# Optimization experiments

Measured on AMD Instinct MI355X. Metric: run time of the kernel, lower is better.

Reference implementation:

```python
import math
import jax, jax.numpy as jnp
import numpy as np

B, T, D = 512, 512, 256
ALPHA = 0.5
BETA = 0.9


def setup_inputs() -> dict:
    key = jax.random.key(0)
    ks = jax.random.split(key, 9)
    s = 1.0 / math.sqrt(D)
    return {
        "window_features": jax.random.normal(ks[0], (B, T, D), jnp.float32),
        "timestamps": jax.random.uniform(ks[1], (B, T), jnp.float32) * 86400.0 * 7,
        "prev_L": jax.random.normal(ks[2], (B, D), jnp.float32),
        "prev_M": jax.random.uniform(ks[3], (B, 1), jnp.float32),
        "pad_mask": jnp.zeros((B, T), jnp.bool_),
        "W_Q": jax.random.normal(ks[4], (D, D), jnp.float32) * s,
        "W_K": jax.random.normal(ks[5], (D, D), jnp.float32) * s,
        "W_V": jax.random.normal(ks[6], (D, D), jnp.float32) * s,
        "cls_w": jax.random.normal(ks[7], (1, 2 * D + 1), jnp.float32) * s,
        "cls_b": jnp.zeros((1,), jnp.float32),
    }


def reference(window_features, timestamps, prev_L, prev_M, pad_mask,
              W_Q, W_K, W_V, cls_w, cls_b):
    Bv, Tv, d = window_features.shape
    valid = ~pad_mask
    valid_f = valid.astype(window_features.dtype)              # [B,T]
    valid_count = jnp.clip(valid_f.sum(1, keepdims=True), 1.0)  # [B,1]

    # decay weights from recency (days)
    t_masked = jnp.where(pad_mask, -1e18, timestamps)
    t_max = t_masked.max(1, keepdims=True)                      # [B,1]
    dt = jnp.clip(t_max - timestamps, 0.0) / 86400.0
    lam = jnp.exp(-ALPHA * dt) * valid_f                        # [B,T]

    # mean-pooled query
    q = (window_features * valid_f[..., None]).sum(1) / valid_count  # [B,d]
    Q = q @ W_Q.T                                               # [B,d]
    K = jnp.einsum('btd,ed->bte', window_features, W_K)         # [B,T,d]
    V = jnp.einsum('btd,ed->bte', window_features, W_V)         # [B,T,d]

    scores = jnp.einsum('bd,btd->bt', Q, K) / math.sqrt(d)      # [B,T]
    scores = jnp.where(pad_mask, -1e9, scores)
    attn = jax.nn.softmax(scores, axis=-1)

    # decay-modulated reweighting + renormalization
    w = lam * attn
    w = w / (w.sum(1, keepdims=True) + 1e-8)

    L_t = jnp.einsum('bt,btd->bd', w, V)                        # [B,d]
    delta_t = L_t - prev_L
    M_t = BETA * prev_M + (1.0 - BETA) * jnp.linalg.norm(delta_t, axis=1, keepdims=True)
    T_event = jnp.concatenate([L_t, delta_t, M_t], axis=-1)     # [B,2d+1]
    p = (T_event @ cls_w.T + cls_b).squeeze(-1)                 # [B]
    return (p, T_event, L_t, M_t)
```

## Files before the change

kernel.cpp:

```cpp
#include <hip/hip_runtime.h>
#include <math.h>

#define ALPHA 0.5f
#define BETA 0.9f
#define Bsz 512
#define Tsz 512
#define Dsz 256
#define TILE 32
#define NTILE (Tsz / TILE)

__device__ __forceinline__ float wave_reduce_sum(float v) {
    v += __shfl_xor(v, 32, 64);
    v += __shfl_xor(v, 16, 64);
    v += __shfl_xor(v, 8, 64);
    v += __shfl_xor(v, 4, 64);
    v += __shfl_xor(v, 2, 64);
    v += __shfl_xor(v, 1, 64);
    return v;
}

__device__ __forceinline__ float wave_reduce_max(float v) {
    v = fmaxf(v, __shfl_xor(v, 32, 64));
    v = fmaxf(v, __shfl_xor(v, 16, 64));
    v = fmaxf(v, __shfl_xor(v, 8, 64));
    v = fmaxf(v, __shfl_xor(v, 4, 64));
    v = fmaxf(v, __shfl_xor(v, 2, 64));
    v = fmaxf(v, __shfl_xor(v, 1, 64));
    return v;
}

__device__ __forceinline__ void load_lds16(const float* g, float* l) {
    __builtin_amdgcn_global_load_lds(
        (const __attribute__((address_space(1))) void*)(g),
        (__attribute__((address_space(3))) void*)(l),
        16, 0, 0);
}

__global__ __launch_bounds__(256) void kA(const float* __restrict__ x,
                                          const float* __restrict__ ts,
                                          const unsigned char* __restrict__ pad,
                                          const float* __restrict__ WQ,
                                          const float* __restrict__ WK,
                                          float* __restrict__ qk,
                                          float* __restrict__ tmax_out) {
    const int b = blockIdx.x;
    const int tid = threadIdx.x;
    const int w = tid >> 6, lane = tid & 63;

    __shared__ float validS[Tsz];
    __shared__ float qpart[4][Dsz];
    __shared__ float qS[Dsz];
    __shared__ float QS[Dsz];
    __shared__ float red[8];
    __shared__ float tmaxS, cntS;

    float lmax = -1e30f;
    float lcnt = 0.f;
    for (int t = tid; t < Tsz; t += 256) {
        bool v = (pad[(size_t)b * Tsz + t] == 0);
        float tv = ts[(size_t)b * Tsz + t];
        validS[t] = v ? 1.f : 0.f;
        if (v) { lmax = fmaxf(lmax, tv); lcnt += 1.f; }
    }
    lmax = wave_reduce_max(lmax);
    lcnt = wave_reduce_sum(lcnt);
    if (lane == 0) { red[w] = lmax; red[4 + w] = lcnt; }
    __syncthreads();
    if (tid == 0) {
        tmaxS = fmaxf(fmaxf(red[0], red[1]), fmaxf(red[2], red[3]));
        cntS = fmaxf(red[4] + red[5] + red[6] + red[7], 1.f);
    }
    __syncthreads();

    const float* xb = x + (size_t)b * Tsz * Dsz;
    float4 a0 = make_float4(0.f, 0.f, 0.f, 0.f);
    float4 a1 = a0, a2 = a0, a3 = a0;
    const int tbase = w * 128;
    for (int i = 0; i < 128; i += 4) {
        const int t = tbase + i;
        float4 x0 = *(const float4*)(xb + (size_t)(t + 0) * Dsz + lane * 4);
        float4 x1 = *(const float4*)(xb + (size_t)(t + 1) * Dsz + lane * 4);
        float4 x2 = *(const float4*)(xb + (size_t)(t + 2) * Dsz + lane * 4);
        float4 x3 = *(const float4*)(xb + (size_t)(t + 3) * Dsz + lane * 4);
        const float v0 = validS[t], v1 = validS[t + 1], v2 = validS[t + 2], v3 = validS[t + 3];
        a0.x += v0 * x0.x; a0.y += v0 * x0.y; a0.z += v0 * x0.z; a0.w += v0 * x0.w;
        a1.x += v1 * x1.x; a1.y += v1 * x1.y; a1.z += v1 * x1.z; a1.w += v1 * x1.w;
        a2.x += v2 * x2.x; a2.y += v2 * x2.y; a2.z += v2 * x2.z; a2.w += v2 * x2.w;
        a3.x += v3 * x3.x; a3.y += v3 * x3.y; a3.z += v3 * x3.z; a3.w += v3 * x3.w;
    }
    float4 accq;
    accq.x = (a0.x + a1.x) + (a2.x + a3.x);
    accq.y = (a0.y + a1.y) + (a2.y + a3.y);
    accq.z = (a0.z + a1.z) + (a2.z + a3.z);
    accq.w = (a0.w + a1.w) + (a2.w + a3.w);
    qpart[w][lane * 4 + 0] = accq.x;
    qpart[w][lane * 4 + 1] = accq.y;
    qpart[w][lane * 4 + 2] = accq.z;
    qpart[w][lane * 4 + 3] = accq.w;
    __syncthreads();
    qS[tid] = (qpart[0][tid] + qpart[1][tid] + qpart[2][tid] + qpart[3][tid]) / cntS;
    __syncthreads();

    float Qi = 0.f;
    const float* wqrow = WQ + (size_t)tid * Dsz;
    #pragma unroll 4
    for (int d4 = 0; d4 < Dsz; d4 += 4) {
        float4 wv = *(const float4*)(wqrow + d4);
        Qi += wv.x * qS[d4] + wv.y * qS[d4 + 1] + wv.z * qS[d4 + 2] + wv.w * qS[d4 + 3];
    }
    QS[tid] = Qi;
    __syncthreads();

    float v = 0.f;
    #pragma unroll 8
    for (int e = 0; e < Dsz; ++e) {
        v += QS[e] * WK[(size_t)e * Dsz + tid];
    }
    qk[(size_t)b * Dsz + tid] = v * 0.0625f;
    if (tid == 0) tmax_out[b] = tmaxS;
}

__global__ __launch_bounds__(256) void kB(const float* __restrict__ x,
                                          const float* __restrict__ ts,
                                          const unsigned char* __restrict__ pad,
                                          const float* __restrict__ qk,
                                          const float* __restrict__ tmax_in,
                                          const float* __restrict__ WV,
                                          const float* __restrict__ prevL,
                                          const float* __restrict__ prevM,
                                          const float* __restrict__ clsw,
                                          const float* __restrict__ clsb,
                                          float* __restrict__ out) {
    const int b = (Bsz - 1) - blockIdx.x;
    const int tid = threadIdx.x;
    const int w = tid >> 6, lane = tid & 63;
    const int rloc = lane >> 3;
    const int sub = lane & 7;

    __shared__ __align__(16) float buf[2][TILE][Dsz];
    __shared__ float lamS[Tsz];
    __shared__ float okS[Tsz];
    __shared__ float gS[TILE];
    __shared__ float accS[4][Dsz];
    __shared__ float EGS[8];
    __shared__ float xwS[Dsz];
    __shared__ float red[4];
    __shared__ float red2[4];

    const float tmax = tmax_in[b];
    for (int t = tid; t < Tsz; t += 256) {
        bool valid = (pad[(size_t)b * Tsz + t] == 0);
        float dt = fmaxf(tmax - ts[(size_t)b * Tsz + t], 0.f) * (1.f / 86400.f);
        lamS[t] = valid ? __expf(-ALPHA * dt) : 0.f;
        okS[t] = valid ? 1.f : 0.f;
    }

    float4 qkr[8];
    #pragma unroll
    for (int jj = 0; jj < 8; ++jj)
        qkr[jj] = *(const float4*)(qk + (size_t)b * Dsz + ((jj * 8 + sub) << 2));

    const float* xb = x + (size_t)b * Tsz * Dsz;

    {
        const int t0 = (NTILE - 1) * TILE;
        #pragma unroll
        for (int k = 0; k < 8; ++k) {
            const int r = w * 8 + k;
            load_lds16(xb + (size_t)(t0 + r) * Dsz + lane * 4, &buf[0][r][0]);
        }
    }
    __syncthreads();

    float4 acc = make_float4(0.f, 0.f, 0.f, 0.f);
    float E = 0.f, G = 0.f;
    int cur = 0;

    for (int it = 0; it < NTILE; ++it) {
        const int tile = (NTILE - 1) - it;

        if (it + 1 < NTILE) {
            const int t0 = (tile - 1) * TILE;
            #pragma unroll
            for (int k = 0; k < 8; ++k) {
                const int r = w * 8 + k;
                load_lds16(xb + (size_t)(t0 + r) * Dsz + lane * 4, &buf[cur ^ 1][r][0]);
            }
        }

        const int r = w * 8 + rloc;
        const float* rowp = &buf[cur][r][0];
        float s = 0.f;
        #pragma unroll
        for (int jj = 0; jj < 8; ++jj) {
            const float4 xv = *(const float4*)(rowp + ((jj * 8 + sub) << 2));
            s += xv.x * qkr[jj].x + xv.y * qkr[jj].y + xv.z * qkr[jj].z + xv.w * qkr[jj].w;
        }
        s += __shfl_xor(s, 1, 64);
        s += __shfl_xor(s, 2, 64);
        s += __shfl_xor(s, 4, 64);
        const int tglob = tile * TILE + r;
        const float e = okS[tglob] * __expf(s);
        const float g = lamS[tglob] * e;
        E += e; G += g;
        if (sub == 0) gS[r] = g;

        #pragma unroll
        for (int k = 0; k < 8; ++k) {
            const float g_k = gS[w * 8 + k];
            const float4 xv = *(const float4*)(&buf[cur][w * 8 + k][lane * 4]);
            acc.x += g_k * xv.x; acc.y += g_k * xv.y; acc.z += g_k * xv.z; acc.w += g_k * xv.w;
        }

        __syncthreads();
        cur ^= 1;
    }

    accS[w][lane * 4 + 0] = acc.x;
    accS[w][lane * 4 + 1] = acc.y;
    accS[w][lane * 4 + 2] = acc.z;
    accS[w][lane * 4 + 3] = acc.w;
    float Ew = wave_reduce_sum(E) * 0.125f;
    float Gw = wave_reduce_sum(G) * 0.125f;
    if (lane == 0) { EGS[w] = Ew; EGS[4 + w] = Gw; }
    __syncthreads();

    {
        float Et = EGS[0] + EGS[1] + EGS[2] + EGS[3];
        float Gt = EGS[4] + EGS[5] + EGS[6] + EGS[7];
        float denom = Gt + 1e-8f * Et;
        float accd = accS[0][tid] + accS[1][tid] + accS[2][tid] + accS[3][tid];
        xwS[tid] = (denom > 0.f) ? accd / denom : 0.f;
    }
    __syncthreads();

    float Le = 0.f;
    const float* wvrow = WV + (size_t)tid * Dsz;
    #pragma unroll 4
    for (int d4 = 0; d4 < Dsz; d4 += 4) {
        float4 wv = *(const float4*)(wvrow + d4);
        Le += wv.x * xwS[d4] + wv.y * xwS[d4 + 1] + wv.z * xwS[d4 + 2] + wv.w * xwS[d4 + 3];
    }
    float delta = Le - prevL[(size_t)b * Dsz + tid];

    float ssq = wave_reduce_sum(delta * delta);
    if (lane == 0) red[w] = ssq;
    __syncthreads();
    float nrm = sqrtf(red[0] + red[1] + red[2] + red[3]);
    float M = BETA * prevM[b] + (1.f - BETA) * nrm;

    float pp = Le * clsw[tid] + delta * clsw[Dsz + tid];
    float psum = wave_reduce_sum(pp);
    if (lane == 0) red2[w] = psum;
    __syncthreads();

    float* out_p = out;
    float* out_T = out + Bsz;
    float* out_L = out + Bsz + (size_t)Bsz * (2 * Dsz + 1);
    float* out_M = out + Bsz + (size_t)Bsz * (2 * Dsz + 1) + (size_t)Bsz * Dsz;

    out_T[(size_t)b * (2 * Dsz + 1) + tid] = Le;
    out_T[(size_t)b * (2 * Dsz + 1) + Dsz + tid] = delta;
    out_L[(size_t)b * Dsz + tid] = Le;
    if (tid == 0) {
        float p = red2[0] + red2[1] + red2[2] + red2[3] + M * clsw[2 * Dsz] + clsb[0];
        out_p[b] = p;
        out_T[(size_t)b * (2 * Dsz + 1) + 2 * Dsz] = M;
        out_M[b] = M;
    }
}

extern "C" void kernel_launch(void* const* d_in, const int* in_sizes, int n_in,
                              void* d_out, int out_size, void* d_ws, size_t ws_size,
                              hipStream_t stream) {
    const float* x     = (const float*)d_in[0];
    const float* ts    = (const float*)d_in[1];
    const float* prevL = (const float*)d_in[2];
    const float* prevM = (const float*)d_in[3];
    const unsigned char* pad = (const unsigned char*)d_in[4];
    const float* WQ    = (const float*)d_in[5];
    const float* WK    = (const float*)d_in[6];
    const float* WV    = (const float*)d_in[7];
    const float* clsw  = (const float*)d_in[8];
    const float* clsb  = (const float*)d_in[9];

    float* ws   = (float*)d_ws;
    float* qk   = ws;
    float* tmax = ws + Bsz * Dsz;

    kA<<<Bsz, 256, 0, stream>>>(x, ts, pad, WQ, WK, qk, tmax);
    kB<<<Bsz, 256, 0, stream>>>(x, ts, pad, qk, tmax, WV, prevL, prevM, clsw, clsb, (float*)d_out);
}
```

Baseline: 453.3 us.

## Fuse query-projection and attention kernels into a single per-batch kernel

Merges the two kernels into one block per batch row. The mean-pooled query, Q and qk vectors are computed into shared memory and used directly, so the workspace round trip and the second launch go away. The x tile prefetch for the attention loop is issued before the Q/K matvecs so the load overlaps that work. The x stream is now read twice within the same block, which may give better L2 reuse. In exchange, the old reversed block order (meant to reuse L2 across kernels) is dropped and per-block latency grows.

Result: faster. 442.2 us (-2.5%).

```diff
diff --git a/kernel.cpp b/kernel.cpp
--- a/kernel.cpp
+++ b/kernel.cpp
@@ -36,22 +36,35 @@
         16, 0, 0);
 }
 
-__global__ __launch_bounds__(256) void kA(const float* __restrict__ x,
-                                          const float* __restrict__ ts,
-                                          const unsigned char* __restrict__ pad,
-                                          const float* __restrict__ WQ,
-                                          const float* __restrict__ WK,
-                                          float* __restrict__ qk,
-                                          float* __restrict__ tmax_out) {
+__global__ __launch_bounds__(256) void fused(const float* __restrict__ x,
+                                             const float* __restrict__ ts,
+                                             const unsigned char* __restrict__ pad,
+                                             const float* __restrict__ WQ,
+                                             const float* __restrict__ WK,
+                                             const float* __restrict__ WV,
+                                             const float* __restrict__ prevL,
+                                             const float* __restrict__ prevM,
+                                             const float* __restrict__ clsw,
+                                             const float* __restrict__ clsb,
+                                             float* __restrict__ out) {
     const int b = blockIdx.x;
     const int tid = threadIdx.x;
     const int w = tid >> 6, lane = tid & 63;
-
-    __shared__ float validS[Tsz];
-    __shared__ float qpart[4][Dsz];
+    const int rloc = lane >> 3;
+    const int sub = lane & 7;
+
+    __shared__ __align__(16) float buf[2][TILE][Dsz];
+    __shared__ float lamS[Tsz];
+    __shared__ float okS[Tsz];
+    __shared__ float part[4][Dsz];
     __shared__ float qS[Dsz];
     __shared__ float QS[Dsz];
+    __shared__ __align__(16) float qkS[Dsz];
+    __shared__ float gS[TILE];
+    __shared__ float xwS[Dsz];
+    __shared__ float EGS[8];
     __shared__ float red[8];
+    __shared__ float red2[4];
     __shared__ float tmaxS, cntS;
 
     float lmax = -1e30f;
@@ -59,7 +72,8 @@
     for (int t = tid; t < Tsz; t += 256) {
         bool v = (pad[(size_t)b * Tsz + t] == 0);
         float tv = ts[(size_t)b * Tsz + t];
-        validS[t] = v ? 1.f : 0.f;
+        okS[t] = v ? 1.f : 0.f;
+        lamS[t] = tv;
         if (v) { lmax = fmaxf(lmax, tv); lcnt += 1.f; }
     }
     lmax = wave_reduce_max(lmax);
@@ -71,6 +85,12 @@
         cntS = fmaxf(red[4] + red[5] + red[6] + red[7], 1.f);
     }
     __syncthreads();
+
+    const float tmax = tmaxS;
+    for (int t = tid; t < Tsz; t += 256) {
+        float dt = fmaxf(tmax - lamS[t], 0.f) * (1.f / 86400.f);
+        lamS[t] = okS[t] * __expf(-ALPHA * dt);
+    }
 
     const float* xb = x + (size_t)b * Tsz * Dsz;
     float4 a0 = make_float4(0.f, 0.f, 0.f, 0.f);
@@ -82,7 +102,7 @@
         float4 x1 = *(const float4*)(xb + (size_t)(t + 1) * Dsz + lane * 4);
         float4 x2 = *(const float4*)(xb + (size_t)(t + 2) * Dsz + lane * 4);
         float4 x3 = *(const float4*)(xb + (size_t)(t + 3) * Dsz + lane * 4);
-        const float v0 = validS[t], v1 = validS[t + 1], v2 = validS[t + 2], v3 = validS[t + 3];
+        const float v0 = okS[t], v1 = okS[t + 1], v2 = okS[t + 2], v3 = okS[t + 3];
         a0.x += v0 * x0.x; a0.y += v0 * x0.y; a0.z += v0 * x0.z; a0.w += v0 * x0.w;
         a1.x += v1 * x1.x; a1.y += v1 * x1.y; a1.z += v1 * x1.z; a1.w += v1 * x1.w;
         a2.x += v2 * x2.x; a2.y += v2 * x2.y; a2.z += v2 * x2.z; a2.w += v2 * x2.w;
@@ -93,12 +113,22 @@
     accq.y = (a0.y + a1.y) + (a2.y + a3.y);
     accq.z = (a0.z + a1.z) + (a2.z + a3.z);
     accq.w = (a0.w + a1.w) + (a2.w + a3.w);
-    qpart[w][lane * 4 + 0] = accq.x;
-    qpart[w][lane * 4 + 1] = accq.y;
-    qpart[w][lane * 4 + 2] = accq.z;
-    qpart[w][lane * 4 + 3] = accq.w;
-    __syncthreads();
-    qS[tid] = (qpart[0][tid] + qpart[1][tid] + qpart[2][tid] + qpart[3][tid]) / cntS;
+    part[w][lane * 4 + 0] = accq.x;
+    part[w][lane * 4 + 1] = accq.y;
+    part[w][lane * 4 + 2] = accq.z;
+    part[w][lane * 4 + 3] = accq.w;
+
+    {
+        const int t0 = (NTILE - 1) * TILE;
+        #pragma unroll
+        for (int k = 0; k < 8; ++k) {
+            const int r = w * 8 + k;
+            load_lds16(xb + (size_t)(t0 + r) * Dsz + lane * 4, &buf[0][r][0]);
+        }
+    }
+    __syncthreads();
+
+    qS[tid] = (part[0][tid] + part[1][tid] + part[2][tid] + part[3][tid]) / cntS;
     __syncthreads();
 
     float Qi = 0.f;
@@ -111,66 +141,23 @@
     QS[tid] = Qi;
     __syncthreads();
 
-    float v = 0.f;
-    #pragma unroll 8
-    for (int e = 0; e < Dsz; ++e) {
-        v += QS[e] * WK[(size_t)e * Dsz + tid];
-    }
-    qk[(size_t)b * Dsz + tid] = v * 0.0625f;
-    if (tid == 0) tmax_out[b] = tmaxS;
-}
-
-__global__ __launch_bounds__(256) void kB(const float* __restrict__ x,
-                                          const float* __restrict__ ts,
-                                          const unsigned char* __restrict__ pad,
-                                          const float* __restrict__ qk,
-                                          const float* __restrict__ tmax_in,
-                                          const float* __restrict__ WV,
-                                          const float* __restrict__ prevL,
-                                          const float* __restrict__ prevM,
-                                          const float* __restrict__ clsw,
-                                          const float* __restrict__ clsb,
-                                          float* __restrict__ out) {
-    const int b = (Bsz - 1) - blockIdx.x;
-    const int tid = threadIdx.x;
-    const int w = tid >> 6, lane = tid & 63;
-    const int rloc = lane >> 3;
-    const int sub = lane & 7;
-
-    __shared__ __align__(16) float buf[2][TILE][Dsz];
-    __shared__ float lamS[Tsz];
-    __shared__ float okS[Tsz];
-    __shared__ float gS[TILE];
-    __shared__ float accS[4][Dsz];
-    __shared__ float EGS[8];
-    __shared__ float xwS[Dsz];
-    __shared__ float red[4];
-    __shared__ float red2[4];
-
-    const float tmax = tmax_in[b];
-    for (int t = tid; t < Tsz; t += 256) {
-        bool valid = (pad[(size_t)b * Tsz + t] == 0);
-        float dt = fmaxf(tmax - ts[(size_t)b * Tsz + t], 0.f) * (1.f / 86400.f);
-        lamS[t] = valid ? __expf(-ALPHA * dt) : 0.f;
-        okS[t] = valid ? 1.f : 0.f;
-    }
+    {
+        float v0 = 0.f, v1 = 0.f, v2 = 0.f, v3 = 0.f;
+        #pragma unroll 4
+        for (int e = 0; e < Dsz; e += 4) {
+            v0 += QS[e + 0] * WK[(size_t)(e + 0) * Dsz + tid];
+            v1 += QS[e + 1] * WK[(size_t)(e + 1) * Dsz + tid];
+            v2 += QS[e + 2] * WK[(size_t)(e + 2) * Dsz + tid];
+            v3 += QS[e + 3] * WK[(size_t)(e + 3) * Dsz + tid];
+        }
+        qkS[tid] = ((v0 + v1) + (v2 + v3)) * 0.0625f;
+    }
+    __syncthreads();
 
     float4 qkr[8];
     #pragma unroll
     for (int jj = 0; jj < 8; ++jj)
-        qkr[jj] = *(const float4*)(qk + (size_t)b * Dsz + ((jj * 8 + sub) << 2));
-
-    const float* xb = x + (size_t)b * Tsz * Dsz;
-
-    {
-        const int t0 = (NTILE - 1) * TILE;
-        #pragma unroll
-        for (int k = 0; k < 8; ++k) {
-            const int r = w * 8 + k;
-            load_lds16(xb + (size_t)(t0 + r) * Dsz + lane * 4, &buf[0][r][0]);
-        }
-    }
-    __syncthreads();
+        qkr[jj] = *(const float4*)(&qkS[(jj * 8 + sub) << 2]);
 
     float4 acc = make_float4(0.f, 0.f, 0.f, 0.f);
     float E = 0.f, G = 0.f;
@@ -216,10 +203,10 @@
         cur ^= 1;
     }
 
-    accS[w][lane * 4 + 0] = acc.x;
-    accS[w][lane * 4 + 1] = acc.y;
-    accS[w][lane * 4 + 2] = acc.z;
-    accS[w][lane * 4 + 3] = acc.w;
+    part[w][lane * 4 + 0] = acc.x;
+    part[w][lane * 4 + 1] = acc.y;
+    part[w][lane * 4 + 2] = acc.z;
+    part[w][lane * 4 + 3] = acc.w;
     float Ew = wave_reduce_sum(E) * 0.125f;
     float Gw = wave_reduce_sum(G) * 0.125f;
     if (lane == 0) { EGS[w] = Ew; EGS[4 + w] = Gw; }
@@ -229,7 +216,7 @@
         float Et = EGS[0] + EGS[1] + EGS[2] + EGS[3];
         float Gt = EGS[4] + EGS[5] + EGS[6] + EGS[7];
         float denom = Gt + 1e-8f * Et;
-        float accd = accS[0][tid] + accS[1][tid] + accS[2][tid] + accS[3][tid];
+        float accd = part[0][tid] + part[1][tid] + part[2][tid] + part[3][tid];
         xwS[tid] = (denom > 0.f) ? accd / denom : 0.f;
     }
     __syncthreads();
@@ -284,10 +271,8 @@
     const float* clsw  = (const float*)d_in[8];
     const float* clsb  = (const float*)d_in[9];
 
-    float* ws   = (float*)d_ws;
-    float* qk   = ws;
-    float* tmax = ws + Bsz * Dsz;
-
-    kA<<<Bsz, 256, 0, stream>>>(x, ts, pad, WQ, WK, qk, tmax);
-    kB<<<Bsz, 256, 0, stream>>>(x, ts, pad, qk, tmax, WV, prevL, prevM, clsw, clsb, (float*)d_out);
-}
+    (void)d_ws; (void)ws_size;
+
+    fused<<<Bsz, 256, 0, stream>>>(x, ts, pad, WQ, WK, WV, prevL, prevM, clsw, clsb,
+                                   (float*)d_out);
+}
```
